# Kernel tuning notes

Hardware: AMD Instinct MI355X
Metric: run time of the kernel (lower is better)

Reference implementation:

```python
import jax, jax.numpy as jnp
import numpy as np

B, T, C, H = 2, 2048, 1024, 16
HS = C // H

def setup_inputs() -> dict:
    key = jax.random.key(0)
    ks = jax.random.split(key, 5)
    s = 0.02
    return {
        "x": jax.random.normal(ks[0], (B, T, C), jnp.float32),
        "W_attn": jax.random.normal(ks[1], (C, 3 * C), jnp.float32) * s,
        "b_attn": jax.random.normal(ks[2], (3 * C,), jnp.float32) * s,
        "W_proj": jax.random.normal(ks[3], (C, C), jnp.float32) * s,
        "b_proj": jax.random.normal(ks[4], (C,), jnp.float32) * s,
    }

def reference(x, W_attn, b_attn, W_proj, b_proj):
    qkv = x @ W_attn + b_attn                      # [B,T,3C]
    q, k, v = jnp.split(qkv, 3, axis=-1)
    # [B,T,C] -> [B,H,T,hs]
    def heads(t):
        return t.reshape(B, T, H, HS).transpose(0, 2, 1, 3)
    q, k, v = heads(q), heads(k), heads(v)
    scale = 1.0 / jnp.sqrt(jnp.asarray(HS, x.dtype))
    attn = jnp.einsum('bhqd,bhkd->bhqk', q, k) * scale
    causal = jnp.tril(jnp.ones((T, T), bool))
    attn = jnp.where(causal[None, None], attn, -jnp.inf)
    attn = jax.nn.softmax(attn, axis=-1)
    y = jnp.einsum('bhqk,bhkd->bhqd', attn, v)
    y = y.transpose(0, 2, 1, 3).reshape(B, T, C)
    return y @ W_proj + b_proj
```

## Files before the change

### kernel.cpp

```cpp
#include <hip/hip_runtime.h>
#include <hip/hip_bf16.h>

static constexpr int Bn = 2, Tn = 2048, Cn = 1024, Hn = 16, HSn = 64;
static constexpr int Mrows = Bn * Tn;
static constexpr size_t PL = (size_t)Bn * Hn * Tn * HSn;

typedef __attribute__((ext_vector_type(8))) short short8;
typedef __attribute__((ext_vector_type(4))) float f32x4;

__device__ __forceinline__ unsigned short f2bf(float f) {
  __hip_bfloat16 h = __float2bfloat16(f);
  return *reinterpret_cast<unsigned short*>(&h);
}

__device__ __forceinline__ float fexp2(float x) {
  return __builtin_amdgcn_exp2f(x);
}

__device__ __forceinline__ void gload_lds16(const void* g, void* l) {
  __builtin_amdgcn_global_load_lds(
      (const __attribute__((address_space(1))) void*)g,
      (__attribute__((address_space(3))) void*)l, 16, 0, 0);
}

#define QSC 0.18033688011112042591999058512524f

__global__ __launch_bounds__(256) void prep_all(
    const float* __restrict__ x, unsigned short* __restrict__ xb,
    const float* __restrict__ Wa, unsigned short* __restrict__ Wab,
    const float* __restrict__ Wp, unsigned short* __restrict__ Wpb)
{
  const int bid = blockIdx.x, tid = threadIdx.x;
  if (bid < 4096) {
    int i = bid * 256 + tid;
    float4 v = ((const float4*)x)[i];
    ushort4 o;
    o.x = f2bf(v.x); o.y = f2bf(v.y); o.z = f2bf(v.z); o.w = f2bf(v.w);
    ((ushort4*)xb)[i] = o;
    return;
  }
  __shared__ float tile[32][33];
  const float* src; unsigned short* dst; int R, Cc, tb;
  if (bid < 4096 + 3072) { src = Wa; dst = Wab; R = Cn; Cc = 3 * Cn; tb = bid - 4096; }
  else                   { src = Wp; dst = Wpb; R = Cn; Cc = Cn;     tb = bid - 4096 - 3072; }
  const int nbx = Cc / 32;
  const int bx = tb % nbx, by = tb / nbx;
  const int tx = tid & 31, ty = tid >> 5;
  const int c0 = bx * 32, r0 = by * 32;
  #pragma unroll
  for (int i = 0; i < 4; ++i)
    tile[ty + 8 * i][tx] = src[(size_t)(r0 + ty + 8 * i) * Cc + c0 + tx];
  __syncthreads();
  #pragma unroll
  for (int i = 0; i < 4; ++i)
    dst[(size_t)(c0 + ty + 8 * i) * R + r0 + tx] = f2bf(tile[tx][ty + 8 * i]);
}

__global__ __launch_bounds__(512) void gemmQKV(
    const unsigned short* __restrict__ A, const unsigned short* __restrict__ Bt,
    const float* __restrict__ bias, unsigned short* __restrict__ qkv, int K)
{
  constexpr int NSTEP = 1024 / 64;
  constexpr int AF = 32;
  constexpr int BF = 24;
  __shared__ alignas(16) unsigned char lds[2][(AF + BF) * 1024];

  const int tid = threadIdx.x, wave = tid >> 6, lane = tid & 63;
  const int wr = wave >> 2, wc = wave & 3;
  const int orig = blockIdx.x;
  const int swz = (orig & 7) * 32 + (orig >> 3);
  const int bx = swz & 15, by = swz >> 4;
  const int tM = by * 256, tN = bx * 192;

  auto STAGE = [&](int buf, int k0) {
    #pragma unroll
    for (int i = 0; i < 7; ++i) {
      int f = wave * 7 + i;
      const unsigned short* g;
      int off;
      if (f < AF) {
        int mg = f >> 1, ks = f & 1;
        g = A + (size_t)(tM + mg * 16 + (lane & 15)) * K + k0 + ks * 32 + (lane >> 4) * 8;
        off = f * 1024;
      } else {
        int fg = f - AF;
        int ng = fg >> 1, ks = fg & 1;
        g = Bt + (size_t)(tN + ng * 16 + (lane & 15)) * K + k0 + ks * 32 + (lane >> 4) * 8;
        off = AF * 1024 + fg * 1024;
      }
      gload_lds16(g, &lds[buf][off]);
    }
  };

  f32x4 acc[8][3] = {};

  STAGE(0, 0);
  STAGE(1, 64);

  for (int t = 0; t < NSTEP; ++t) {
    if (t == NSTEP - 1)
      asm volatile("s_waitcnt vmcnt(0)" ::: "memory");
    else
      asm volatile("s_waitcnt vmcnt(7)" ::: "memory");
    __builtin_amdgcn_s_barrier();

    const int cur = t & 1;
    short8 af[8][2], bfr[3][2];
    #pragma unroll
    for (int ks = 0; ks < 2; ++ks) {
      #pragma unroll
      for (int m = 0; m < 8; ++m)
        af[m][ks] = *(const short8*)&lds[cur][((wr * 8 + m) * 2 + ks) * 1024 + lane * 16];
      #pragma unroll
      for (int n = 0; n < 3; ++n)
        bfr[n][ks] = *(const short8*)&lds[cur][AF * 1024 + ((wc * 3 + n) * 2 + ks) * 1024 + lane * 16];
    }
    asm volatile("s_waitcnt lgkmcnt(0)" ::: "memory");
    __builtin_amdgcn_sched_barrier(0);
    __builtin_amdgcn_s_barrier();

    if (t + 2 < NSTEP) STAGE(cur, (t + 2) * 64);

    __builtin_amdgcn_s_setprio(1);
    #pragma unroll
    for (int ks = 0; ks < 2; ++ks)
      #pragma unroll
      for (int m = 0; m < 8; ++m)
        #pragma unroll
        for (int n = 0; n < 3; ++n)
          acc[m][n] = __builtin_amdgcn_mfma_f32_16x16x32_bf16(af[m][ks], bfr[n][ks], acc[m][n], 0, 0, 0);
    __builtin_amdgcn_s_setprio(0);
  }

  const int a = lane & 15, hq = lane >> 4;
  #pragma unroll
  for (int m = 0; m < 8; ++m) {
    #pragma unroll
    for (int n = 0; n < 3; ++n) {
      int c = tN + wc * 48 + n * 16 + a;
      float bv = bias[c];
      int which = c >> 10;
      int cc = c & 1023, hh = cc >> 6, d = cc & 63;
      int row0 = tM + wr * 128 + m * 16 + hq * 4;
      int b = row0 >> 11, t0 = row0 & 2047;
      int bh = b * Hn + hh;
      if (which == 2) {
        ushort4 pk;
        pk.x = f2bf(acc[m][n][0] + bv);
        pk.y = f2bf(acc[m][n][1] + bv);
        pk.z = f2bf(acc[m][n][2] + bv);
        pk.w = f2bf(acc[m][n][3] + bv);
        *(ushort4*)&qkv[2 * PL + ((size_t)bh * HSn + d) * Tn + t0] = pk;
      } else {
        float sc = (which == 0) ? QSC : 1.0f;
        #pragma unroll
        for (int r = 0; r < 4; ++r) {
          float v = (acc[m][n][r] + bv) * sc;
          qkv[(size_t)which * PL + ((size_t)bh * Tn + t0 + r) * HSn + d] = f2bf(v);
        }
      }
    }
  }
}

template <int WM, int WN>
__global__ __launch_bounds__(256) void gemmP(
    const unsigned short* __restrict__ A, const unsigned short* __restrict__ Bt,
    const float* __restrict__ bias, float* __restrict__ O, int N, int K)
{
  constexpr int BM = WM * 32, BNt = WN * 32;
  constexpr int AF = BM / 16;
  constexpr int BF = BNt / 16;
  constexpr int NF = AF + BF;
  constexpr int PW = NF / 4;
  static_assert(PW == 3, "vmcnt literal");
  __shared__ alignas(16) unsigned char lds[2][NF * 1024];

  const int tid = threadIdx.x, wave = tid >> 6, lane = tid & 63;
  const int wr = wave >> 1, wc = wave & 1;
  const int tM = blockIdx.y * BM, tN = blockIdx.x * BNt;

  auto STAGE = [&](int buf, int k0) {
    #pragma unroll
    for (int i = 0; i < PW; ++i) {
      int f = wave * PW + i;
      const unsigned short* g;
      if (f < AF)
        g = A + (size_t)(tM + f * 16 + (lane & 15)) * K + k0 + (lane >> 4) * 8;
      else
        g = Bt + (size_t)(tN + (f - AF) * 16 + (lane & 15)) * K + k0 + (lane >> 4) * 8;
      gload_lds16(g, &lds[buf][f * 1024]);
    }
  };

  f32x4 acc[WM][WN] = {};

  STAGE(0, 0);
  for (int t = 0, k0 = 0;; ++t, k0 += 32) {
    const int cur = t & 1;
    if (k0 + 32 < K) {
      STAGE(cur ^ 1, k0 + 32);
      asm volatile("s_waitcnt vmcnt(3)" ::: "memory");
    } else {
      asm volatile("s_waitcnt vmcnt(0)" ::: "memory");
    }
    __builtin_amdgcn_s_barrier();

    short8 af[WM], bfr[WN];
    #pragma unroll
    for (int m = 0; m < WM; ++m)
      af[m] = *(const short8*)&lds[cur][(wr * WM + m) * 1024 + lane * 16];
    #pragma unroll
    for (int n = 0; n < WN; ++n)
      bfr[n] = *(const short8*)&lds[cur][(AF + wc * WN + n) * 1024 + lane * 16];
    #pragma unroll
    for (int m = 0; m < WM; ++m)
      #pragma unroll
      for (int n = 0; n < WN; ++n)
        acc[m][n] = __builtin_amdgcn_mfma_f32_16x16x32_bf16(af[m], bfr[n], acc[m][n], 0, 0, 0);

    __builtin_amdgcn_s_barrier();
    if (k0 + 32 >= K) break;
  }

  const int a = lane & 15, hq = lane >> 4;
  #pragma unroll
  for (int m = 0; m < WM; ++m) {
    #pragma unroll
    for (int n = 0; n < WN; ++n) {
      int c = tN + wc * (WN * 16) + n * 16 + a;
      float bv = bias[c];
      int r0 = tM + wr * (WM * 16) + m * 16 + hq * 4;
      #pragma unroll
      for (int r = 0; r < 4; ++r)
        O[(size_t)(r0 + r) * N + c] = acc[m][n][r] + bv;
    }
  }
}

__global__ __launch_bounds__(256) void attn_mfma(
    const unsigned short* __restrict__ Qg, const unsigned short* __restrict__ Kg,
    const unsigned short* __restrict__ Vtg, unsigned short* __restrict__ Y)
{
  __shared__ alignas(16) unsigned char lds[50176];
  const int bh = blockIdx.x;
  const int yb = blockIdx.y;
  const int tid = threadIdx.x, wave = tid >> 6, lane = tid & 63;
  const int a = lane & 15, h = lane >> 4;
  const unsigned short* Qp = Qg + (size_t)bh * Tn * HSn;
  const unsigned short* Kp = Kg + (size_t)bh * Tn * HSn;
  const unsigned short* Vp = Vtg + (size_t)bh * HSn * Tn;
  const int pbase = 40960 + wave * 2304;
  const int qglob = wave * 16 + a;
  const int b = bh >> 4, hd = bh & 15;

  auto STAGE_K = [&](int kb, int kv0) {
    #pragma unroll
    for (int i = 0; i < 2; ++i) {
      int r8 = wave * 16 + i * 8;
      int row = r8 + (lane >> 3);
      int ch = (lane & 7) ^ (row & 7);
      gload_lds16(Kp + (size_t)(kv0 + row) * HSn + ch * 8,
                  &lds[8192 + kb * 8192 + r8 * 128]);
    }
  };
  auto STAGE_V = [&](int vb, int kv0) {
    #pragma unroll
    for (int i = 0; i < 2; ++i) {
      int r8 = wave * 16 + i * 8;
      int row = r8 + (lane >> 3);
      int ch = (lane & 7) ^ (row & 7);
      gload_lds16(Vp + (size_t)row * Tn + kv0 + ch * 8,
                  &lds[24576 + vb * 8192 + r8 * 128]);
    }
  };

  short8 ones;
  #pragma unroll
  for (int j = 0; j < 8; ++j) ones[j] = (short)0x3F80;

  for (int ph = 0; ph < 2; ++ph) {
    const int qt = ph ? (31 - yb) : yb;
    const int q0 = qt * 64;

    #pragma unroll
    for (int i = 0; i < 2; ++i) {
      int r8 = wave * 16 + i * 8;
      int row = r8 + (lane >> 3);
      int ch = (lane & 7) ^ (row & 7);
      gload_lds16(Qp + (size_t)(q0 + row) * HSn + ch * 8, &lds[r8 * 128]);
    }
    STAGE_K(0, 0);
    STAGE_V(0, 0);
    if (qt >= 1) {
      STAGE_K(1, 64);
      STAGE_V(1, 64);
      asm volatile("s_waitcnt vmcnt(8)" ::: "memory");
    } else {
      asm volatile("s_waitcnt vmcnt(4)" ::: "memory");
    }

    short8 qf[2];
    #pragma unroll
    for (int ks = 0; ks < 2; ++ks) {
      int row = wave * 16 + a;
      int ch = (ks * 4 + h) ^ (row & 7);
      qf[ks] = *(const short8*)&lds[row * 128 + ch * 16];
    }

    f32x4 o[4] = {};
    f32x4 lacc = {};

    for (int t = 0; t <= qt; ++t) {
      const int kb = t & 1;
      if (t == qt)
        asm volatile("s_waitcnt vmcnt(0)" ::: "memory");
      else
        asm volatile("s_waitcnt vmcnt(4)" ::: "memory");
      __builtin_amdgcn_s_barrier();

      const int kbase = 8192 + kb * 8192;
      const int vbase = 24576 + kb * 8192;

      f32x4 s[4] = {};
      __builtin_amdgcn_s_setprio(1);
      #pragma unroll
      for (int ks = 0; ks < 2; ++ks)
        #pragma unroll
        for (int n = 0; n < 4; ++n) {
          int kr = n * 16 + a;
          int ch = (ks * 4 + h) ^ (kr & 7);
          short8 kf = *(const short8*)&lds[kbase + kr * 128 + ch * 16];
          s[n] = __builtin_amdgcn_mfma_f32_16x16x32_bf16(kf, qf[ks], s[n], 0, 0, 0);
        }
      __builtin_amdgcn_s_setprio(0);

      if (t == qt) {
        #pragma unroll
        for (int n = 0; n < 4; ++n)
          #pragma unroll
          for (int r = 0; r < 4; ++r)
            if ((n * 16 + h * 4 + r) > qglob) s[n][r] = -1e30f;
      }

      #pragma unroll
      for (int n = 0; n < 4; ++n)
        #pragma unroll
        for (int r = 0; r < 4; ++r) s[n][r] = fexp2(s[n][r]);

      #pragma unroll
      for (int n = 0; n < 4; ++n) {
        uint2 w2;
        w2.x = (unsigned)f2bf(s[n][0]) | ((unsigned)f2bf(s[n][1]) << 16);
        w2.y = (unsigned)f2bf(s[n][2]) | ((unsigned)f2bf(s[n][3]) << 16);
        *(uint2*)&lds[pbase + (a * 36 + n * 8 + h * 2) * 4] = w2;
      }

      __builtin_amdgcn_s_setprio(1);
      #pragma unroll
      for (int ks = 0; ks < 2; ++ks) {
        short8 pa = *(const short8*)&lds[pbase + (a * 36 + ks * 16 + h * 4) * 4];
        lacc = __builtin_amdgcn_mfma_f32_16x16x32_bf16(pa, ones, lacc, 0, 0, 0);
        #pragma unroll
        for (int n = 0; n < 4; ++n) {
          int d = n * 16 + a;
          int ch = (ks * 4 + h) ^ (d & 7);
          short8 vf = *(const short8*)&lds[vbase + d * 128 + ch * 16];
          o[n] = __builtin_amdgcn_mfma_f32_16x16x32_bf16(pa, vf, o[n], 0, 0, 0);
        }
      }
      __builtin_amdgcn_s_setprio(0);

      __builtin_amdgcn_s_barrier();
      if (t + 2 <= qt) {
        STAGE_K(kb, (t + 2) * 64);
        STAGE_V(kb, (t + 2) * 64);
      }
    }

    f32x4 inv;
    #pragma unroll
    for (int r = 0; r < 4; ++r) inv[r] = 1.0f / lacc[r];
    #pragma unroll
    for (int n = 0; n < 4; ++n)
      #pragma unroll
      for (int r = 0; r < 4; ++r) {
        int tr = q0 + wave * 16 + 4 * h + r;
        int col = hd * 64 + n * 16 + a;
        Y[((size_t)(b * Tn + tr)) * Cn + col] = f2bf(o[n][r] * inv[r]);
      }
  }
}

extern "C" void kernel_launch(void* const* d_in, const int* in_sizes, int n_in,
                              void* d_out, int out_size, void* d_ws, size_t ws_size,
                              hipStream_t stream) {
  const float* x      = (const float*)d_in[0];
  const float* W_attn = (const float*)d_in[1];
  const float* b_attn = (const float*)d_in[2];
  const float* W_proj = (const float*)d_in[3];
  const float* b_proj = (const float*)d_in[4];
  float* out = (float*)d_out;

  unsigned short* xb  = (unsigned short*)d_ws;
  unsigned short* Wab = xb + (size_t)Mrows * Cn;
  unsigned short* Wpb = Wab + (size_t)3 * Cn * Cn;
  unsigned short* qkv = Wpb + (size_t)Cn * Cn;
  unsigned short* y   = qkv + 3 * PL;

  prep_all<<<4096 + 3072 + 1024, 256, 0, stream>>>(x, xb, W_attn, Wab, W_proj, Wpb);

  gemmQKV<<<256, 512, 0, stream>>>(xb, Wab, b_attn, qkv, Cn);

  attn_mfma<<<dim3(Bn * Hn, 16), 256, 0, stream>>>(qkv, qkv + PL, qkv + 2 * PL, y);

  gemmP<4, 2><<<dim3(Cn / 64, Mrows / 128), 256, 0, stream>>>(
      y, Wpb, b_proj, out, Cn, Cn);
}
```

Baseline: 108.6 us.

## Use 4-stage K=32 LDS pipeline with split A/B loader waves in QKV GEMM

The QKV GEMM main loop moves from a 2-buffer, K=64-per-step pipeline to a 4-buffer ring with K=32 steps and three stages in flight. Waves 0-3 now load only A fragments and waves 4-7 only B fragments, so per-wave vmcnt waits are set to match. The second barrier per iteration, the explicit lgkmcnt wait and the setprio hints are removed. The aim is deeper load latency hiding and less barrier overhead per step, at the cost of more loop iterations, fewer MFMAs per step, and uneven load work across waves. Overwriting buffer (t+3)&3 after a single barrier relies on every wave having finished reading it in the previous iteration.

```diff
diff --git a/kernel.cpp b/kernel.cpp
--- a/kernel.cpp
+++ b/kernel.cpp
@@ -60,10 +60,11 @@
     const unsigned short* __restrict__ A, const unsigned short* __restrict__ Bt,
     const float* __restrict__ bias, unsigned short* __restrict__ qkv, int K)
 {
-  constexpr int NSTEP = 1024 / 64;
-  constexpr int AF = 32;
-  constexpr int BF = 24;
-  __shared__ alignas(16) unsigned char lds[2][(AF + BF) * 1024];
+  constexpr int NSTEP = 32;
+  constexpr int AF = 16;
+  constexpr int BF = 12;
+  constexpr int FB = (AF + BF) * 1024;
+  __shared__ alignas(16) unsigned char lds[4][FB];
 
   const int tid = threadIdx.x, wave = tid >> 6, lane = tid & 63;
   const int wr = wave >> 2, wc = wave & 3;
@@ -73,63 +74,59 @@
   const int tM = by * 256, tN = bx * 192;
 
   auto STAGE = [&](int buf, int k0) {
-    #pragma unroll
-    for (int i = 0; i < 7; ++i) {
-      int f = wave * 7 + i;
-      const unsigned short* g;
-      int off;
-      if (f < AF) {
-        int mg = f >> 1, ks = f & 1;
-        g = A + (size_t)(tM + mg * 16 + (lane & 15)) * K + k0 + ks * 32 + (lane >> 4) * 8;
-        off = f * 1024;
-      } else {
-        int fg = f - AF;
-        int ng = fg >> 1, ks = fg & 1;
-        g = Bt + (size_t)(tN + ng * 16 + (lane & 15)) * K + k0 + ks * 32 + (lane >> 4) * 8;
-        off = AF * 1024 + fg * 1024;
-      }
-      gload_lds16(g, &lds[buf][off]);
+    if (wave < 4) {
+      #pragma unroll
+      for (int i = 0; i < 4; ++i) {
+        int f = wave * 4 + i;
+        const unsigned short* g =
+            A + (size_t)(tM + f * 16 + (lane & 15)) * K + k0 + (lane >> 4) * 8;
+        gload_lds16(g, &lds[buf][f * 1024]);
+      }
+    } else {
+      #pragma unroll
+      for (int i = 0; i < 3; ++i) {
+        int fg = (wave - 4) * 3 + i;
+        const unsigned short* g =
+            Bt + (size_t)(tN + fg * 16 + (lane & 15)) * K + k0 + (lane >> 4) * 8;
+        gload_lds16(g, &lds[buf][AF * 1024 + fg * 1024]);
+      }
     }
   };
 
   f32x4 acc[8][3] = {};
 
   STAGE(0, 0);
-  STAGE(1, 64);
+  STAGE(1, 32);
+  STAGE(2, 64);
 
   for (int t = 0; t < NSTEP; ++t) {
-    if (t == NSTEP - 1)
-      asm volatile("s_waitcnt vmcnt(0)" ::: "memory");
-    else
-      asm volatile("s_waitcnt vmcnt(7)" ::: "memory");
+    const int ahead = NSTEP - 1 - t;
+    if (wave < 4) {
+      if (ahead >= 2)      asm volatile("s_waitcnt vmcnt(8)" ::: "memory");
+      else if (ahead == 1) asm volatile("s_waitcnt vmcnt(4)" ::: "memory");
+      else                 asm volatile("s_waitcnt vmcnt(0)" ::: "memory");
+    } else {
+      if (ahead >= 2)      asm volatile("s_waitcnt vmcnt(6)" ::: "memory");
+      else if (ahead == 1) asm volatile("s_waitcnt vmcnt(3)" ::: "memory");
+      else                 asm volatile("s_waitcnt vmcnt(0)" ::: "memory");
+    }
     __builtin_amdgcn_s_barrier();
 
-    const int cur = t & 1;
-    short8 af[8][2], bfr[3][2];
-    #pragma unroll
-    for (int ks = 0; ks < 2; ++ks) {
-      #pragma unroll
-      for (int m = 0; m < 8; ++m)
-        af[m][ks] = *(const short8*)&lds[cur][((wr * 8 + m) * 2 + ks) * 1024 + lane * 16];
+    if (t + 3 < NSTEP) STAGE((t + 3) & 3, (t + 3) * 32);
+
+    const unsigned char* base = lds[t & 3];
+    short8 af[8], bfr[3];
+    #pragma unroll
+    for (int m = 0; m < 8; ++m)
+      af[m] = *(const short8*)&base[(wr * 8 + m) * 1024 + lane * 16];
+    #pragma unroll
+    for (int n = 0; n < 3; ++n)
+      bfr[n] = *(const short8*)&base[AF * 1024 + (wc * 3 + n) * 1024 + lane * 16];
+    #pragma unroll
+    for (int m = 0; m < 8; ++m)
       #pragma unroll
       for (int n = 0; n < 3; ++n)
-        bfr[n][ks] = *(const short8*)&lds[cur][AF * 1024 + ((wc * 3 + n) * 2 + ks) * 1024 + lane * 16];
-    }
-    asm volatile("s_waitcnt lgkmcnt(0)" ::: "memory");
-    __builtin_amdgcn_sched_barrier(0);
-    __builtin_amdgcn_s_barrier();
-
-    if (t + 2 < NSTEP) STAGE(cur, (t + 2) * 64);
-
-    __builtin_amdgcn_s_setprio(1);
-    #pragma unroll
-    for (int ks = 0; ks < 2; ++ks)
-      #pragma unroll
-      for (int m = 0; m < 8; ++m)
-        #pragma unroll
-        for (int n = 0; n < 3; ++n)
-          acc[m][n] = __builtin_amdgcn_mfma_f32_16x16x32_bf16(af[m][ks], bfr[n][ks], acc[m][n], 0, 0, 0);
-    __builtin_amdgcn_s_setprio(0);
+        acc[m][n] = __builtin_amdgcn_mfma_f32_16x16x32_bf16(af[m], bfr[n], acc[m][n], 0, 0, 0);
   }
 
   const int a = lane & 15, hq = lane >> 4;
```

New measurement: 108.5 us. Within noise of the previous version (-0.1%).

## Enlarge QKV GEMM tile to 256x256 and interleave staging with MFMA groups

Applied to the files above, without the earlier changes.

The QKV projection GEMM tile grows from 256x192 to 256x256, giving each wave 8x4 accumulators and a 192-block grid instead of 256. The K loop is split into four sub-groups, each of which issues part of the next tile's global-to-LDS loads between MFMA batches. Each wave now waits for all outstanding loads at the start of every step, so only one step of prefetch is in flight. The larger tile cuts redundant A and B traffic, but 192 blocks leave some of the 256 CUs idle, and the extra barriers plus 128KB of LDS per block may hurt latency hiding.

```diff
diff --git a/kernel.cpp b/kernel.cpp
--- a/kernel.cpp
+++ b/kernel.cpp
@@ -60,84 +60,92 @@
     const unsigned short* __restrict__ A, const unsigned short* __restrict__ Bt,
     const float* __restrict__ bias, unsigned short* __restrict__ qkv, int K)
 {
-  constexpr int NSTEP = 1024 / 64;
-  constexpr int AF = 32;
-  constexpr int BF = 24;
-  __shared__ alignas(16) unsigned char lds[2][(AF + BF) * 1024];
+  constexpr int NT = 16;
+  __shared__ alignas(16) unsigned char lds[2][65536];
 
   const int tid = threadIdx.x, wave = tid >> 6, lane = tid & 63;
   const int wr = wave >> 2, wc = wave & 3;
   const int orig = blockIdx.x;
-  const int swz = (orig & 7) * 32 + (orig >> 3);
-  const int bx = swz & 15, by = swz >> 4;
-  const int tM = by * 256, tN = bx * 192;
-
-  auto STAGE = [&](int buf, int k0) {
-    #pragma unroll
-    for (int i = 0; i < 7; ++i) {
-      int f = wave * 7 + i;
-      const unsigned short* g;
-      int off;
-      if (f < AF) {
-        int mg = f >> 1, ks = f & 1;
-        g = A + (size_t)(tM + mg * 16 + (lane & 15)) * K + k0 + ks * 32 + (lane >> 4) * 8;
-        off = f * 1024;
+  const int swz = (orig & 7) * 24 + (orig >> 3);
+  const int bx = swz % 12, by = swz / 12;
+  const int tM = by * 256, tN = bx * 256;
+
+  auto STAGE_GRP = [&](int buf, int k0, int grp) {
+    const int ks = grp & 1;
+    #pragma unroll
+    for (int i = 0; i < 2; ++i) {
+      int fr = wave * 2 + i;
+      if (grp < 2) {
+        const unsigned short* g =
+            Bt + (size_t)(tN + fr * 16 + (lane & 15)) * K + k0 + ks * 32 + (lane >> 4) * 8;
+        gload_lds16(g, &lds[buf][32768 + (fr * 2 + ks) * 1024]);
       } else {
-        int fg = f - AF;
-        int ng = fg >> 1, ks = fg & 1;
-        g = Bt + (size_t)(tN + ng * 16 + (lane & 15)) * K + k0 + ks * 32 + (lane >> 4) * 8;
-        off = AF * 1024 + fg * 1024;
-      }
-      gload_lds16(g, &lds[buf][off]);
+        const unsigned short* g =
+            A + (size_t)(tM + fr * 16 + (lane & 15)) * K + k0 + ks * 32 + (lane >> 4) * 8;
+        gload_lds16(g, &lds[buf][(fr * 2 + ks) * 1024]);
+      }
     }
   };
 
-  f32x4 acc[8][3] = {};
-
-  STAGE(0, 0);
-  STAGE(1, 64);
-
-  for (int t = 0; t < NSTEP; ++t) {
-    if (t == NSTEP - 1)
+  f32x4 acc[8][4] = {};
+
+  #pragma unroll
+  for (int g = 0; g < 4; ++g) STAGE_GRP(0, 0, g);
+  #pragma unroll
+  for (int g = 0; g < 4; ++g) STAGE_GRP(1, 64, g);
+
+  for (int t = 0; t < NT; ++t) {
+    if (t == 0)
+      asm volatile("s_waitcnt vmcnt(8)" ::: "memory");
+    else
       asm volatile("s_waitcnt vmcnt(0)" ::: "memory");
-    else
-      asm volatile("s_waitcnt vmcnt(7)" ::: "memory");
     __builtin_amdgcn_s_barrier();
 
-    const int cur = t & 1;
-    short8 af[8][2], bfr[3][2];
-    #pragma unroll
-    for (int ks = 0; ks < 2; ++ks) {
-      #pragma unroll
-      for (int m = 0; m < 8; ++m)
-        af[m][ks] = *(const short8*)&lds[cur][((wr * 8 + m) * 2 + ks) * 1024 + lane * 16];
-      #pragma unroll
-      for (int n = 0; n < 3; ++n)
-        bfr[n][ks] = *(const short8*)&lds[cur][AF * 1024 + ((wc * 3 + n) * 2 + ks) * 1024 + lane * 16];
-    }
-    asm volatile("s_waitcnt lgkmcnt(0)" ::: "memory");
-    __builtin_amdgcn_sched_barrier(0);
-    __builtin_amdgcn_s_barrier();
-
-    if (t + 2 < NSTEP) STAGE(cur, (t + 2) * 64);
-
-    __builtin_amdgcn_s_setprio(1);
-    #pragma unroll
-    for (int ks = 0; ks < 2; ++ks)
-      #pragma unroll
-      for (int m = 0; m < 8; ++m)
-        #pragma unroll
-        for (int n = 0; n < 3; ++n)
-          acc[m][n] = __builtin_amdgcn_mfma_f32_16x16x32_bf16(af[m][ks], bfr[n][ks], acc[m][n], 0, 0, 0);
-    __builtin_amdgcn_s_setprio(0);
+    const int buf = t & 1;
+    const unsigned char* base = lds[buf];
+    const bool dostage = (t >= 1 && t < NT - 1);
+    const int k1 = (t + 1) * 64;
+
+    short8 bfr[4][2];
+    #pragma unroll
+    for (int q = 0; q < 4; ++q) {
+      short8 af[2][2];
+      #pragma unroll
+      for (int j = 0; j < 2; ++j)
+        #pragma unroll
+        for (int ks = 0; ks < 2; ++ks)
+          af[j][ks] = *(const short8*)&base[((wr * 8 + q * 2 + j) * 2 + ks) * 1024 + lane * 16];
+      if (q == 0) {
+        #pragma unroll
+        for (int n = 0; n < 4; ++n)
+          #pragma unroll
+          for (int ks = 0; ks < 2; ++ks)
+            bfr[n][ks] = *(const short8*)&base[32768 + ((wc * 4 + n) * 2 + ks) * 1024 + lane * 16];
+      }
+      if (dostage) STAGE_GRP(buf ^ 1, k1, q);
+
+      __builtin_amdgcn_s_barrier();
+      asm volatile("s_waitcnt lgkmcnt(0)" ::: "memory");
+      __builtin_amdgcn_s_setprio(1);
+      #pragma unroll
+      for (int ks = 0; ks < 2; ++ks)
+        #pragma unroll
+        for (int j = 0; j < 2; ++j)
+          #pragma unroll
+          for (int n = 0; n < 4; ++n)
+            acc[q * 2 + j][n] = __builtin_amdgcn_mfma_f32_16x16x32_bf16(
+                af[j][ks], bfr[n][ks], acc[q * 2 + j][n], 0, 0, 0);
+      __builtin_amdgcn_s_setprio(0);
+      __builtin_amdgcn_s_barrier();
+    }
   }
 
   const int a = lane & 15, hq = lane >> 4;
   #pragma unroll
   for (int m = 0; m < 8; ++m) {
     #pragma unroll
-    for (int n = 0; n < 3; ++n) {
-      int c = tN + wc * 48 + n * 16 + a;
+    for (int n = 0; n < 4; ++n) {
+      int c = tN + wc * 64 + n * 16 + a;
       float bv = bias[c];
       int which = c >> 10;
       int cc = c & 1023, hh = cc >> 6, d = cc & 63;
@@ -410,7 +418,7 @@
 
   prep_all<<<4096 + 3072 + 1024, 256, 0, stream>>>(x, xb, W_attn, Wab, W_proj, Wpb);
 
-  gemmQKV<<<256, 512, 0, stream>>>(xb, Wab, b_attn, qkv, Cn);
+  gemmQKV<<<192, 512, 0, stream>>>(xb, Wab, b_attn, qkv, Cn);
 
   attn_mfma<<<dim3(Bn * Hn, 16), 256, 0, stream>>>(qkv, qkv + PL, qkv + 2 * PL, y);
 
```

After: 120.0 us. +10.6%, slower.

## Shrink QKV GEMM tile to 128x192 with 4 waves and K-step 32

Applied to the files above, without the earlier changes.

The QKV GEMM moves from 256x192 tiles with 8 waves and a 64-wide K step to 128x192 tiles with 4 waves and a 32-wide K step, launching 512 blocks instead of 256. The prefetch schedule also changes from two-deep staging to single-ahead double buffering, and the separate LDS-wait sched barrier is dropped. The aim is better CU coverage on a many-CU GPU and a smaller LDS footprint, at the cost of less data reuse per tile and twice as many K iterations, each with two barriers.

```diff
diff --git a/kernel.cpp b/kernel.cpp
--- a/kernel.cpp
+++ b/kernel.cpp
@@ -56,92 +56,77 @@
     dst[(size_t)(c0 + ty + 8 * i) * R + r0 + tx] = f2bf(tile[tx][ty + 8 * i]);
 }
 
-__global__ __launch_bounds__(512) void gemmQKV(
+__global__ __launch_bounds__(256) void gemmQKV(
     const unsigned short* __restrict__ A, const unsigned short* __restrict__ Bt,
     const float* __restrict__ bias, unsigned short* __restrict__ qkv, int K)
 {
-  constexpr int NSTEP = 1024 / 64;
-  constexpr int AF = 32;
-  constexpr int BF = 24;
-  __shared__ alignas(16) unsigned char lds[2][(AF + BF) * 1024];
+  constexpr int AF = 8;
+  constexpr int BF = 12;
+  constexpr int NF = AF + BF;
+  __shared__ alignas(16) unsigned char lds[2][NF * 1024];
 
   const int tid = threadIdx.x, wave = tid >> 6, lane = tid & 63;
-  const int wr = wave >> 2, wc = wave & 3;
+  const int wr = wave >> 1, wc = wave & 1;
   const int orig = blockIdx.x;
-  const int swz = (orig & 7) * 32 + (orig >> 3);
+  const int swz = (orig & 7) * 64 + (orig >> 3);
   const int bx = swz & 15, by = swz >> 4;
-  const int tM = by * 256, tN = bx * 192;
+  const int tM = by * 128, tN = bx * 192;
 
   auto STAGE = [&](int buf, int k0) {
     #pragma unroll
-    for (int i = 0; i < 7; ++i) {
-      int f = wave * 7 + i;
+    for (int i = 0; i < 5; ++i) {
+      int f = wave * 5 + i;
       const unsigned short* g;
-      int off;
-      if (f < AF) {
-        int mg = f >> 1, ks = f & 1;
-        g = A + (size_t)(tM + mg * 16 + (lane & 15)) * K + k0 + ks * 32 + (lane >> 4) * 8;
-        off = f * 1024;
-      } else {
-        int fg = f - AF;
-        int ng = fg >> 1, ks = fg & 1;
-        g = Bt + (size_t)(tN + ng * 16 + (lane & 15)) * K + k0 + ks * 32 + (lane >> 4) * 8;
-        off = AF * 1024 + fg * 1024;
-      }
-      gload_lds16(g, &lds[buf][off]);
+      if (f < AF)
+        g = A + (size_t)(tM + f * 16 + (lane & 15)) * K + k0 + (lane >> 4) * 8;
+      else
+        g = Bt + (size_t)(tN + (f - AF) * 16 + (lane & 15)) * K + k0 + (lane >> 4) * 8;
+      gload_lds16(g, &lds[buf][f * 1024]);
     }
   };
 
-  f32x4 acc[8][3] = {};
+  f32x4 acc[4][6] = {};
 
   STAGE(0, 0);
-  STAGE(1, 64);
-
-  for (int t = 0; t < NSTEP; ++t) {
-    if (t == NSTEP - 1)
+  for (int t = 0, k0 = 0;; ++t, k0 += 32) {
+    const int cur = t & 1;
+    if (k0 + 32 < K) {
+      STAGE(cur ^ 1, k0 + 32);
+      asm volatile("s_waitcnt vmcnt(5)" ::: "memory");
+    } else {
       asm volatile("s_waitcnt vmcnt(0)" ::: "memory");
-    else
-      asm volatile("s_waitcnt vmcnt(7)" ::: "memory");
+    }
     __builtin_amdgcn_s_barrier();
 
-    const int cur = t & 1;
-    short8 af[8][2], bfr[3][2];
-    #pragma unroll
-    for (int ks = 0; ks < 2; ++ks) {
-      #pragma unroll
-      for (int m = 0; m < 8; ++m)
-        af[m][ks] = *(const short8*)&lds[cur][((wr * 8 + m) * 2 + ks) * 1024 + lane * 16];
-      #pragma unroll
-      for (int n = 0; n < 3; ++n)
-        bfr[n][ks] = *(const short8*)&lds[cur][AF * 1024 + ((wc * 3 + n) * 2 + ks) * 1024 + lane * 16];
-    }
-    asm volatile("s_waitcnt lgkmcnt(0)" ::: "memory");
-    __builtin_amdgcn_sched_barrier(0);
+    short8 af[4], bfr[6];
+    #pragma unroll
+    for (int m = 0; m < 4; ++m)
+      af[m] = *(const short8*)&lds[cur][(wr * 4 + m) * 1024 + lane * 16];
+    #pragma unroll
+    for (int n = 0; n < 6; ++n)
+      bfr[n] = *(const short8*)&lds[cur][(AF + wc * 6 + n) * 1024 + lane * 16];
+    __builtin_amdgcn_s_setprio(1);
+    #pragma unroll
+    for (int m = 0; m < 4; ++m)
+      #pragma unroll
+      for (int n = 0; n < 6; ++n)
+        acc[m][n] = __builtin_amdgcn_mfma_f32_16x16x32_bf16(af[m], bfr[n], acc[m][n], 0, 0, 0);
+    __builtin_amdgcn_s_setprio(0);
+
     __builtin_amdgcn_s_barrier();
-
-    if (t + 2 < NSTEP) STAGE(cur, (t + 2) * 64);
-
-    __builtin_amdgcn_s_setprio(1);
-    #pragma unroll
-    for (int ks = 0; ks < 2; ++ks)
-      #pragma unroll
-      for (int m = 0; m < 8; ++m)
-        #pragma unroll
-        for (int n = 0; n < 3; ++n)
-          acc[m][n] = __builtin_amdgcn_mfma_f32_16x16x32_bf16(af[m][ks], bfr[n][ks], acc[m][n], 0, 0, 0);
-    __builtin_amdgcn_s_setprio(0);
+    if (k0 + 32 >= K) break;
   }
 
   const int a = lane & 15, hq = lane >> 4;
   #pragma unroll
-  for (int m = 0; m < 8; ++m) {
-    #pragma unroll
-    for (int n = 0; n < 3; ++n) {
-      int c = tN + wc * 48 + n * 16 + a;
+  for (int m = 0; m < 4; ++m) {
+    #pragma unroll
+    for (int n = 0; n < 6; ++n) {
+      int c = tN + wc * 96 + n * 16 + a;
       float bv = bias[c];
       int which = c >> 10;
       int cc = c & 1023, hh = cc >> 6, d = cc & 63;
-      int row0 = tM + wr * 128 + m * 16 + hq * 4;
+      int row0 = tM + wr * 64 + m * 16 + hq * 4;
       int b = row0 >> 11, t0 = row0 & 2047;
       int bh = b * Hn + hh;
       if (which == 2) {
@@ -410,7 +395,7 @@
 
   prep_all<<<4096 + 3072 + 1024, 256, 0, stream>>>(x, xb, W_attn, Wab, W_proj, Wpb);
 
-  gemmQKV<<<256, 512, 0, stream>>>(xb, Wab, b_attn, qkv, Cn);
+  gemmQKV<<<512, 256, 0, stream>>>(xb, Wab, b_attn, qkv, Cn);
 
   attn_mfma<<<dim3(Bn * Hn, 16), 256, 0, stream>>>(qkv, qkv + PL, qkv + 2 * PL, y);
 
```

New measurement: 117.7 us. 8.4% more time.
